# Performance work log

Hardware: AMD Instinct MI355X
Metric: run time of the kernel (lower is better)

Reference implementation:

```python
import jax, jax.numpy as jnp
import numpy as np

HIDDEN = 2048
NUM_HEADS = 16
HEAD_DIM = HIDDEN // NUM_HEADS
BATCH, SEQ = 2, 2048


def setup_inputs() -> dict:
    key = jax.random.key(0)
    ks = jax.random.split(key, 9)
    s = 1.0 / np.sqrt(HIDDEN)
    return {
        "hidden_state": jax.random.normal(ks[0], (BATCH, SEQ, HIDDEN), dtype=jnp.float32),
        "Wq": jax.random.normal(ks[1], (HIDDEN, HIDDEN), dtype=jnp.float32) * s,
        "bq": jax.random.normal(ks[2], (HIDDEN,), dtype=jnp.float32) * 0.01,
        "Wk": jax.random.normal(ks[3], (HIDDEN, HIDDEN), dtype=jnp.float32) * s,
        "bk": jax.random.normal(ks[4], (HIDDEN,), dtype=jnp.float32) * 0.01,
        "Wv": jax.random.normal(ks[5], (HIDDEN, HIDDEN), dtype=jnp.float32) * s,
        "bv": jax.random.normal(ks[6], (HIDDEN,), dtype=jnp.float32) * 0.01,
        "Wo": jax.random.normal(ks[7], (HIDDEN, HIDDEN), dtype=jnp.float32) * s,
        "bo": jax.random.normal(ks[8], (HIDDEN,), dtype=jnp.float32) * 0.01,
    }


def _split_heads(x):
    # (B, S, H*D) -> (B, H, S, D)
    b, s, _ = x.shape
    return x.reshape(b, s, NUM_HEADS, HEAD_DIM).transpose(0, 2, 1, 3)


def reference(hidden_state, Wq, bq, Wk, bk, Wv, bv, Wo, bo):
    q = _split_heads(hidden_state @ Wq + bq)
    k = _split_heads(hidden_state @ Wk + bk)
    v = _split_heads(hidden_state @ Wv + bv)
    scale = 1.0 / jnp.sqrt(jnp.asarray(HEAD_DIM, dtype=hidden_state.dtype))
    scores = jnp.einsum("bhqd,bhkd->bhqk", q, k) * scale  # (B,H,S,S)
    probs = jax.nn.softmax(scores, axis=-1)
    out = jnp.einsum("bhqk,bhkd->bhqd", probs, v)  # (B,H,S,D)
    b, h, s, d = out.shape
    out = out.transpose(0, 2, 1, 3).reshape(b, s, h * d)  # merge heads
    return out @ Wo + bo
```

## Files before the change

### kernel.cpp

```cpp
#include <hip/hip_runtime.h>
#include <math.h>

typedef __bf16 bf16;
typedef __bf16 bf16x4 __attribute__((ext_vector_type(4)));
typedef __bf16 bf16x8 __attribute__((ext_vector_type(8)));
typedef float  f32x4  __attribute__((ext_vector_type(4)));

#define HIDDEN 2048
#define NH     16
#define HD     128
#define BATCH  2
#define SEQ    2048
#define MROWS  (BATCH*SEQ)
#define NQKV   (3*HIDDEN)

__device__ __forceinline__ void async16(const bf16* g, bf16* l) {
  __builtin_amdgcn_global_load_lds(
      (const __attribute__((address_space(1))) void*)g,
      (__attribute__((address_space(3))) void*)l, 16, 0, 0);
}

__global__ __launch_bounds__(256) void cast_f32_bf16_kernel(
    const float* __restrict__ src, bf16* __restrict__ dst, int n4) {
  int i = blockIdx.x * 256 + threadIdx.x;
  if (i >= n4) return;
  float4 f = ((const float4*)src)[i];
  bf16x4 o;
  o[0] = (bf16)f.x; o[1] = (bf16)f.y; o[2] = (bf16)f.z; o[3] = (bf16)f.w;
  ((bf16x4*)dst)[i] = o;
}

__global__ __launch_bounds__(256) void transpose_cast_kernel(
    const float* __restrict__ src, bf16* __restrict__ dst) {
  __shared__ float t[32][33];
  int x  = blockIdx.x * 32 + threadIdx.x;
  int y0 = blockIdx.y * 32;
#pragma unroll
  for (int i = 0; i < 32; i += 8)
    t[threadIdx.y + i][threadIdx.x] = src[(size_t)(y0 + threadIdx.y + i) * HIDDEN + x];
  __syncthreads();
  int xo  = blockIdx.y * 32 + threadIdx.x;
  int yo0 = blockIdx.x * 32;
#pragma unroll
  for (int i = 0; i < 32; i += 8)
    dst[(size_t)(yo0 + threadIdx.y + i) * HIDDEN + xo] = (bf16)t[threadIdx.x][threadIdx.y + i];
}

__global__ __launch_bounds__(256) void concat3_kernel(
    const float* __restrict__ a, const float* __restrict__ b,
    const float* __restrict__ c, float* __restrict__ dst) {
  int i = blockIdx.x * 256 + threadIdx.x;
  float v = (i < 2048) ? a[i] : (i < 4096 ? b[i - 2048] : c[i - 4096]);
  dst[i] = v;
}

__global__ __launch_bounds__(256) void transpose_v_kernel(
    const bf16* __restrict__ QKV, bf16* __restrict__ Vt) {
  __shared__ bf16 t[32][33];
  int bh = blockIdx.z, b = bh >> 4, h = bh & 15;
  const bf16* src = QKV + (size_t)b * SEQ * NQKV + 2 * HIDDEN + h * HD;
  bf16* dst = Vt + (size_t)bh * HD * SEQ;
  int s0 = blockIdx.x * 32, d0 = blockIdx.y * 32;
#pragma unroll
  for (int i = 0; i < 32; i += 8)
    t[threadIdx.y + i][threadIdx.x] = src[(size_t)(s0 + threadIdx.y + i) * NQKV + d0 + threadIdx.x];
  __syncthreads();
#pragma unroll
  for (int i = 0; i < 32; i += 8)
    dst[(size_t)(d0 + threadIdx.y + i) * SEQ + s0 + threadIdx.x] = t[threadIdx.x][threadIdx.y + i];
}

template <typename OutT>
__global__ __launch_bounds__(256) void gemm_bt_bias(
    const bf16* __restrict__ A, const bf16* __restrict__ Bt,
    const float* __restrict__ bias, OutT* __restrict__ C, int N, int K) {
  __shared__ bf16 Ash[128 * 32];
  __shared__ bf16 Bsh[128 * 32];
  const int tid = threadIdx.x;
  const int wave = tid >> 6, lane = tid & 63, quad = lane >> 4, l16 = lane & 15;
  const int wm = (wave & 1) * 64, wn = (wave >> 1) * 64;
  const int m0 = blockIdx.x * 128, n0 = blockIdx.y * 128;
  (void)lane;

  const f32x4 zero4 = {0.f, 0.f, 0.f, 0.f};
  f32x4 acc[4][4];
#pragma unroll
  for (int i = 0; i < 4; i++)
#pragma unroll
    for (int j = 0; j < 4; j++) acc[i][j] = zero4;

  const int crow = tid >> 2, ccc = tid & 3;

  for (int kt = 0; kt < K; kt += 32) {
    __syncthreads();
    async16(&A[(size_t)(m0 + crow) * K + kt + ccc * 8],       &Ash[crow * 32 + ccc * 8]);
    async16(&A[(size_t)(m0 + crow + 64) * K + kt + ccc * 8],  &Ash[(crow + 64) * 32 + ccc * 8]);
    async16(&Bt[(size_t)(n0 + crow) * K + kt + ccc * 8],      &Bsh[crow * 32 + ccc * 8]);
    async16(&Bt[(size_t)(n0 + crow + 64) * K + kt + ccc * 8], &Bsh[(crow + 64) * 32 + ccc * 8]);
    __syncthreads();

    bf16x8 af[4], bfr[4];
#pragma unroll
    for (int i = 0; i < 4; i++) af[i]  = *(const bf16x8*)&Ash[(wm + i * 16 + l16) * 32 + quad * 8];
#pragma unroll
    for (int j = 0; j < 4; j++) bfr[j] = *(const bf16x8*)&Bsh[(wn + j * 16 + l16) * 32 + quad * 8];
#pragma unroll
    for (int i = 0; i < 4; i++)
#pragma unroll
      for (int j = 0; j < 4; j++)
        acc[i][j] = __builtin_amdgcn_mfma_f32_16x16x32_bf16(af[i], bfr[j], acc[i][j], 0, 0, 0);
  }

#pragma unroll
  for (int i = 0; i < 4; i++)
#pragma unroll
    for (int j = 0; j < 4; j++) {
      int n = n0 + wn + j * 16 + l16;
      float bv = bias[n];
#pragma unroll
      for (int r = 0; r < 4; r++) {
        int m = m0 + wm + i * 16 + quad * 4 + r;
        C[(size_t)m * N + n] = (OutT)(acc[i][j][r] + bv);
      }
    }
}

#define KTS   64
#define PPAD  72

__global__ __launch_bounds__(256, 2) void flash_attn_kernel(
    const bf16* __restrict__ QKV, const bf16* __restrict__ Vt, bf16* __restrict__ O) {
  const int bh = blockIdx.y, b = bh >> 4, h = bh & 15;
  const int q0 = blockIdx.x * 128;
  const int tid = threadIdx.x, wave = tid >> 6, lane = tid & 63, quad = lane >> 4, l16 = lane & 15;

  const bf16* Qb  = QKV + (size_t)b * SEQ * NQKV + h * HD;
  const bf16* Kb  = QKV + (size_t)b * SEQ * NQKV + HIDDEN + h * HD;
  const bf16* Vtb = Vt + (size_t)bh * HD * SEQ;

  __shared__ bf16 Ksh[KTS * HD];
  __shared__ bf16 Vsh[HD * KTS];
  __shared__ bf16 Psh[128 * PPAD];

  const int qrow = q0 + wave * 32;
  const float sc = 0.08838834764831845f * 1.44269504088896340f;

  bf16x8 qf[2][4];
#pragma unroll
  for (int mt = 0; mt < 2; mt++)
#pragma unroll
    for (int kk = 0; kk < 4; kk++) {
      bf16x8 t = *(const bf16x8*)&Qb[(size_t)(qrow + mt * 16 + l16) * NQKV + kk * 32 + quad * 8];
#pragma unroll
      for (int j = 0; j < 8; j++) t[j] = (bf16)((float)t[j] * sc);
      qf[mt][kk] = t;
    }

  const f32x4 zero4 = {0.f, 0.f, 0.f, 0.f};
  f32x4 oacc[2][8];
#pragma unroll
  for (int mt = 0; mt < 2; mt++)
#pragma unroll
    for (int nt = 0; nt < 8; nt++) oacc[mt][nt] = zero4;

  float lrun[2][4];
#pragma unroll
  for (int mt = 0; mt < 2; mt++)
#pragma unroll
    for (int r = 0; r < 4; r++) lrun[mt][r] = 0.f;

  const int krp = tid >> 4, kpp = tid & 15;
  const int vrp = tid >> 3, vpp = tid & 7;
  const int l7 = l16 & 7;

  for (int kt = 0; kt < SEQ; kt += KTS) {
    __syncthreads();
#pragma unroll
    for (int s = 0; s < 4; s++) {
      int r  = s * 16 + krp;
      int c  = kpp ^ (r & 7);
      async16(&Kb[(size_t)(kt + r) * NQKV + c * 8], &Ksh[s * 2048 + tid * 8]);
      int rv = s * 32 + vrp;
      int cv = vpp ^ (rv & 7);
      async16(&Vtb[(size_t)rv * SEQ + kt + cv * 8], &Vsh[s * 2048 + tid * 8]);
    }
    __syncthreads();

    f32x4 sacc[2][4];
#pragma unroll
    for (int mt = 0; mt < 2; mt++)
#pragma unroll
      for (int nt = 0; nt < 4; nt++) sacc[mt][nt] = zero4;
#pragma unroll
    for (int kk = 0; kk < 4; kk++) {
      bf16x8 kf[4];
#pragma unroll
      for (int nt = 0; nt < 4; nt++) {
        int p = (4 * kk + quad) ^ l7;
        kf[nt] = *(const bf16x8*)&Ksh[(nt * 16 + l16) * HD + p * 8];
      }
#pragma unroll
      for (int mt = 0; mt < 2; mt++)
#pragma unroll
        for (int nt = 0; nt < 4; nt++)
          sacc[mt][nt] = __builtin_amdgcn_mfma_f32_16x16x32_bf16(qf[mt][kk], kf[nt], sacc[mt][nt], 0, 0, 0);
    }

    float rs[2][4] = {};
#pragma unroll
    for (int mt = 0; mt < 2; mt++)
#pragma unroll
      for (int nt = 0; nt < 4; nt++)
#pragma unroll
        for (int r = 0; r < 4; r++) {
          float p = exp2f(sacc[mt][nt][r]);
          rs[mt][r] += p;
          Psh[(wave * 32 + mt * 16 + quad * 4 + r) * PPAD + nt * 16 + l16] = (bf16)p;
        }
#pragma unroll
    for (int mt = 0; mt < 2; mt++)
#pragma unroll
      for (int r = 0; r < 4; r++) {
        float t = rs[mt][r];
        t += __shfl_xor(t, 1);
        t += __shfl_xor(t, 2);
        t += __shfl_xor(t, 4);
        t += __shfl_xor(t, 8);
        lrun[mt][r] += t;
      }

#pragma unroll
    for (int kk2 = 0; kk2 < 2; kk2++) {
      bf16x8 pf[2], vf[8];
#pragma unroll
      for (int mt = 0; mt < 2; mt++)
        pf[mt] = *(const bf16x8*)&Psh[(wave * 32 + mt * 16 + l16) * PPAD + kk2 * 32 + quad * 8];
#pragma unroll
      for (int nt = 0; nt < 8; nt++) {
        int p = (4 * kk2 + quad) ^ l7;
        vf[nt] = *(const bf16x8*)&Vsh[(nt * 16 + l16) * KTS + p * 8];
      }
#pragma unroll
      for (int mt = 0; mt < 2; mt++)
#pragma unroll
        for (int nt = 0; nt < 8; nt++)
          oacc[mt][nt] = __builtin_amdgcn_mfma_f32_16x16x32_bf16(pf[mt], vf[nt], oacc[mt][nt], 0, 0, 0);
    }
  }

#pragma unroll
  for (int mt = 0; mt < 2; mt++) {
    float inv[4];
#pragma unroll
    for (int r = 0; r < 4; r++) inv[r] = 1.0f / lrun[mt][r];
#pragma unroll
    for (int nt = 0; nt < 8; nt++)
#pragma unroll
      for (int r = 0; r < 4; r++) {
        int q = qrow + mt * 16 + quad * 4 + r;
        int d = nt * 16 + l16;
        O[(size_t)(b * SEQ + q) * HIDDEN + h * HD + d] = (bf16)(oacc[mt][nt][r] * inv[r]);
      }
  }
}

extern "C" void kernel_launch(void* const* d_in, const int* in_sizes, int n_in,
                              void* d_out, int out_size, void* d_ws, size_t ws_size,
                              hipStream_t stream) {
  const float* hs = (const float*)d_in[0];
  const float* Wq = (const float*)d_in[1];
  const float* bq = (const float*)d_in[2];
  const float* Wk = (const float*)d_in[3];
  const float* bk = (const float*)d_in[4];
  const float* Wv = (const float*)d_in[5];
  const float* bv = (const float*)d_in[6];
  const float* Wo = (const float*)d_in[7];
  const float* bo = (const float*)d_in[8];
  float* out = (float*)d_out;

  char* ws = (char*)d_ws;
  bf16*  Abf   = (bf16*)(ws);
  bf16*  WtQKV = (bf16*)(ws + 16777216);
  bf16*  WtO   = (bf16*)(ws + 41943040);
  float* biasQ = (float*)(ws + 50331648);
  bf16*  QKV   = (bf16*)(ws + 50356224);
  bf16*  VT    = (bf16*)(ws + 100687872);
  bf16*  Obf   = (bf16*)(ws + 117465088);

  dim3 tb(32, 8);
  cast_f32_bf16_kernel<<<8192, 256, 0, stream>>>(hs, Abf, 2097152);
  transpose_cast_kernel<<<dim3(64, 64), tb, 0, stream>>>(Wq, WtQKV);
  transpose_cast_kernel<<<dim3(64, 64), tb, 0, stream>>>(Wk, WtQKV + 2048 * 2048);
  transpose_cast_kernel<<<dim3(64, 64), tb, 0, stream>>>(Wv, WtQKV + 2 * 2048 * 2048);
  transpose_cast_kernel<<<dim3(64, 64), tb, 0, stream>>>(Wo, WtO);
  concat3_kernel<<<24, 256, 0, stream>>>(bq, bk, bv, biasQ);

  gemm_bt_bias<bf16><<<dim3(32, 48), 256, 0, stream>>>(Abf, WtQKV, biasQ, QKV, NQKV, HIDDEN);
  transpose_v_kernel<<<dim3(64, 4, 32), tb, 0, stream>>>(QKV, VT);
  flash_attn_kernel<<<dim3(16, 32), 256, 0, stream>>>(QKV, VT, Obf);
  gemm_bt_bias<float><<<dim3(32, 16), 256, 0, stream>>>(Obf, WtO, bo, out, HIDDEN, HIDDEN);
}
```

Before: 466.7 us.

## Use 32x32 MFMA with swizzled LDS in GEMM, XCD block mapping, smaller attention tiles

The GEMM switches from 16x16x32 to 32x32x16 MFMA tiles and XOR-swizzles the LDS layout to avoid bank conflicts. It also remaps the linear block index so each XCD handles a contiguous range of N-blocks for better L2 reuse. The flash attention kernel halves its query tile to 64 rows, one 16-row strip per wave, doubling the grid and raising occupancy to 3 blocks per CU. The four weight transpose launches are merged into one launch. The smaller attention tile means each loaded K/V tile is reused across fewer queries, which raises K/V load traffic.

New measurement: 483.2 us. 3.5% more time.

```diff
diff --git a/kernel.cpp b/kernel.cpp
--- a/kernel.cpp
+++ b/kernel.cpp
@@ -5,6 +5,7 @@
 typedef __bf16 bf16x4 __attribute__((ext_vector_type(4)));
 typedef __bf16 bf16x8 __attribute__((ext_vector_type(8)));
 typedef float  f32x4  __attribute__((ext_vector_type(4)));
+typedef float  f32x16 __attribute__((ext_vector_type(16)));
 
 #define HIDDEN 2048
 #define NH     16
@@ -30,8 +31,18 @@
   ((bf16x4*)dst)[i] = o;
 }
 
-__global__ __launch_bounds__(256) void transpose_cast_kernel(
-    const float* __restrict__ src, bf16* __restrict__ dst) {
+__global__ __launch_bounds__(256) void transpose_cast4_kernel(
+    const float* __restrict__ s0, const float* __restrict__ s1,
+    const float* __restrict__ s2, const float* __restrict__ s3,
+    bf16* __restrict__ d0, bf16* __restrict__ d1,
+    bf16* __restrict__ d2, bf16* __restrict__ d3) {
+  const float* src; bf16* dst;
+  switch (blockIdx.z) {
+    case 0: src = s0; dst = d0; break;
+    case 1: src = s1; dst = d1; break;
+    case 2: src = s2; dst = d2; break;
+    default: src = s3; dst = d3; break;
+  }
   __shared__ float t[32][33];
   int x  = blockIdx.x * 32 + threadIdx.x;
   int y0 = blockIdx.y * 32;
@@ -77,50 +88,63 @@
   __shared__ bf16 Ash[128 * 32];
   __shared__ bf16 Bsh[128 * 32];
   const int tid = threadIdx.x;
-  const int wave = tid >> 6, lane = tid & 63, quad = lane >> 4, l16 = lane & 15;
+  const int wave = tid >> 6, lane = tid & 63;
+  const int l32 = lane & 31, lhi = lane >> 5;
   const int wm = (wave & 1) * 64, wn = (wave >> 1) * 64;
-  const int m0 = blockIdx.x * 128, n0 = blockIdx.y * 128;
-  (void)lane;
-
-  const f32x4 zero4 = {0.f, 0.f, 0.f, 0.f};
-  f32x4 acc[4][4];
-#pragma unroll
-  for (int i = 0; i < 4; i++)
-#pragma unroll
-    for (int j = 0; j < 4; j++) acc[i][j] = zero4;
+
+  const int NB = N >> 7;
+  const int bid = blockIdx.x;
+  const int xcd = bid & 7, jj = bid >> 3;
+  const int nb = xcd * (NB >> 3) + (jj >> 5);
+  const int mb = jj & 31;
+  const int m0 = mb * 128, n0 = nb * 128;
+
+  f32x16 acc[2][2];
+#pragma unroll
+  for (int i = 0; i < 2; i++)
+#pragma unroll
+    for (int j = 0; j < 2; j++)
+#pragma unroll
+      for (int r = 0; r < 16; r++) acc[i][j][r] = 0.f;
 
   const int crow = tid >> 2, ccc = tid & 3;
+  const int cs = ccc ^ (crow & 3);
 
   for (int kt = 0; kt < K; kt += 32) {
     __syncthreads();
-    async16(&A[(size_t)(m0 + crow) * K + kt + ccc * 8],       &Ash[crow * 32 + ccc * 8]);
-    async16(&A[(size_t)(m0 + crow + 64) * K + kt + ccc * 8],  &Ash[(crow + 64) * 32 + ccc * 8]);
-    async16(&Bt[(size_t)(n0 + crow) * K + kt + ccc * 8],      &Bsh[crow * 32 + ccc * 8]);
-    async16(&Bt[(size_t)(n0 + crow + 64) * K + kt + ccc * 8], &Bsh[(crow + 64) * 32 + ccc * 8]);
-    __syncthreads();
-
-    bf16x8 af[4], bfr[4];
-#pragma unroll
-    for (int i = 0; i < 4; i++) af[i]  = *(const bf16x8*)&Ash[(wm + i * 16 + l16) * 32 + quad * 8];
-#pragma unroll
-    for (int j = 0; j < 4; j++) bfr[j] = *(const bf16x8*)&Bsh[(wn + j * 16 + l16) * 32 + quad * 8];
-#pragma unroll
-    for (int i = 0; i < 4; i++)
-#pragma unroll
-      for (int j = 0; j < 4; j++)
-        acc[i][j] = __builtin_amdgcn_mfma_f32_16x16x32_bf16(af[i], bfr[j], acc[i][j], 0, 0, 0);
-  }
-
-#pragma unroll
-  for (int i = 0; i < 4; i++)
-#pragma unroll
-    for (int j = 0; j < 4; j++) {
-      int n = n0 + wn + j * 16 + l16;
+    async16(&A[(size_t)(m0 + crow) * K + kt + cs * 8],       &Ash[tid * 8]);
+    async16(&A[(size_t)(m0 + crow + 64) * K + kt + cs * 8],  &Ash[2048 + tid * 8]);
+    async16(&Bt[(size_t)(n0 + crow) * K + kt + cs * 8],      &Bsh[tid * 8]);
+    async16(&Bt[(size_t)(n0 + crow + 64) * K + kt + cs * 8], &Bsh[2048 + tid * 8]);
+    __syncthreads();
+
+#pragma unroll
+    for (int s = 0; s < 2; s++) {
+      const int p = (s * 2 + lhi) ^ (l32 & 3);
+      bf16x8 af[2], bfr[2];
+#pragma unroll
+      for (int i = 0; i < 2; i++) {
+        af[i]  = *(const bf16x8*)&Ash[(wm + i * 32 + l32) * 32 + p * 8];
+        bfr[i] = *(const bf16x8*)&Bsh[(wn + i * 32 + l32) * 32 + p * 8];
+      }
+#pragma unroll
+      for (int i = 0; i < 2; i++)
+#pragma unroll
+        for (int j = 0; j < 2; j++)
+          acc[i][j] = __builtin_amdgcn_mfma_f32_32x32x16_bf16(af[i], bfr[j], acc[i][j], 0, 0, 0);
+    }
+  }
+
+#pragma unroll
+  for (int i = 0; i < 2; i++)
+#pragma unroll
+    for (int j = 0; j < 2; j++) {
+      int n = n0 + wn + j * 32 + l32;
       float bv = bias[n];
 #pragma unroll
-      for (int r = 0; r < 4; r++) {
-        int m = m0 + wm + i * 16 + quad * 4 + r;
-        C[(size_t)m * N + n] = (OutT)(acc[i][j][r] + bv);
+      for (int r = 0; r < 16; r++) {
+        int row = wm + i * 32 + (r & 3) + 8 * (r >> 2) + 4 * lhi;
+        C[(size_t)(m0 + row) * N + n] = (OutT)(acc[i][j][r] + bv);
       }
     }
 }
@@ -128,10 +152,10 @@
 #define KTS   64
 #define PPAD  72
 
-__global__ __launch_bounds__(256, 2) void flash_attn_kernel(
+__global__ __launch_bounds__(256, 3) void flash_attn_kernel(
     const bf16* __restrict__ QKV, const bf16* __restrict__ Vt, bf16* __restrict__ O) {
   const int bh = blockIdx.y, b = bh >> 4, h = bh & 15;
-  const int q0 = blockIdx.x * 128;
+  const int q0 = blockIdx.x * 64;
   const int tid = threadIdx.x, wave = tid >> 6, lane = tid & 63, quad = lane >> 4, l16 = lane & 15;
 
   const bf16* Qb  = QKV + (size_t)b * SEQ * NQKV + h * HD;
@@ -140,34 +164,25 @@
 
   __shared__ bf16 Ksh[KTS * HD];
   __shared__ bf16 Vsh[HD * KTS];
-  __shared__ bf16 Psh[128 * PPAD];
-
-  const int qrow = q0 + wave * 32;
+  __shared__ bf16 Psh[64 * PPAD];
+
+  const int qrow = q0 + wave * 16;
   const float sc = 0.08838834764831845f * 1.44269504088896340f;
 
-  bf16x8 qf[2][4];
-#pragma unroll
-  for (int mt = 0; mt < 2; mt++)
-#pragma unroll
-    for (int kk = 0; kk < 4; kk++) {
-      bf16x8 t = *(const bf16x8*)&Qb[(size_t)(qrow + mt * 16 + l16) * NQKV + kk * 32 + quad * 8];
-#pragma unroll
-      for (int j = 0; j < 8; j++) t[j] = (bf16)((float)t[j] * sc);
-      qf[mt][kk] = t;
-    }
+  bf16x8 qf[4];
+#pragma unroll
+  for (int kk = 0; kk < 4; kk++) {
+    bf16x8 t = *(const bf16x8*)&Qb[(size_t)(qrow + l16) * NQKV + kk * 32 + quad * 8];
+#pragma unroll
+    for (int j = 0; j < 8; j++) t[j] = (bf16)((float)t[j] * sc);
+    qf[kk] = t;
+  }
 
   const f32x4 zero4 = {0.f, 0.f, 0.f, 0.f};
-  f32x4 oacc[2][8];
-#pragma unroll
-  for (int mt = 0; mt < 2; mt++)
-#pragma unroll
-    for (int nt = 0; nt < 8; nt++) oacc[mt][nt] = zero4;
-
-  float lrun[2][4];
-#pragma unroll
-  for (int mt = 0; mt < 2; mt++)
-#pragma unroll
-    for (int r = 0; r < 4; r++) lrun[mt][r] = 0.f;
+  f32x4 oacc[8];
+#pragma unroll
+  for (int nt = 0; nt < 8; nt++) oacc[nt] = zero4;
+  float lrun[4] = {0.f, 0.f, 0.f, 0.f};
 
   const int krp = tid >> 4, kpp = tid & 15;
   const int vrp = tid >> 3, vpp = tid & 7;
@@ -186,82 +201,65 @@
     }
     __syncthreads();
 
-    f32x4 sacc[2][4];
-#pragma unroll
-    for (int mt = 0; mt < 2; mt++)
-#pragma unroll
-      for (int nt = 0; nt < 4; nt++) sacc[mt][nt] = zero4;
+    f32x4 sacc[4];
+#pragma unroll
+    for (int nt = 0; nt < 4; nt++) sacc[nt] = zero4;
 #pragma unroll
     for (int kk = 0; kk < 4; kk++) {
+      const int p = (4 * kk + quad) ^ l7;
       bf16x8 kf[4];
 #pragma unroll
-      for (int nt = 0; nt < 4; nt++) {
-        int p = (4 * kk + quad) ^ l7;
+      for (int nt = 0; nt < 4; nt++)
         kf[nt] = *(const bf16x8*)&Ksh[(nt * 16 + l16) * HD + p * 8];
+#pragma unroll
+      for (int nt = 0; nt < 4; nt++)
+        sacc[nt] = __builtin_amdgcn_mfma_f32_16x16x32_bf16(qf[kk], kf[nt], sacc[nt], 0, 0, 0);
+    }
+
+    float rs[4] = {0.f, 0.f, 0.f, 0.f};
+#pragma unroll
+    for (int nt = 0; nt < 4; nt++)
+#pragma unroll
+      for (int r = 0; r < 4; r++) {
+        float p = exp2f(sacc[nt][r]);
+        rs[r] += p;
+        Psh[(wave * 16 + quad * 4 + r) * PPAD + nt * 16 + l16] = (bf16)p;
       }
 #pragma unroll
-      for (int mt = 0; mt < 2; mt++)
-#pragma unroll
-        for (int nt = 0; nt < 4; nt++)
-          sacc[mt][nt] = __builtin_amdgcn_mfma_f32_16x16x32_bf16(qf[mt][kk], kf[nt], sacc[mt][nt], 0, 0, 0);
-    }
-
-    float rs[2][4] = {};
-#pragma unroll
-    for (int mt = 0; mt < 2; mt++)
-#pragma unroll
-      for (int nt = 0; nt < 4; nt++)
-#pragma unroll
-        for (int r = 0; r < 4; r++) {
-          float p = exp2f(sacc[mt][nt][r]);
-          rs[mt][r] += p;
-          Psh[(wave * 32 + mt * 16 + quad * 4 + r) * PPAD + nt * 16 + l16] = (bf16)p;
-        }
-#pragma unroll
-    for (int mt = 0; mt < 2; mt++)
-#pragma unroll
-      for (int r = 0; r < 4; r++) {
-        float t = rs[mt][r];
-        t += __shfl_xor(t, 1);
-        t += __shfl_xor(t, 2);
-        t += __shfl_xor(t, 4);
-        t += __shfl_xor(t, 8);
-        lrun[mt][r] += t;
-      }
+    for (int r = 0; r < 4; r++) {
+      float t = rs[r];
+      t += __shfl_xor(t, 1);
+      t += __shfl_xor(t, 2);
+      t += __shfl_xor(t, 4);
+      t += __shfl_xor(t, 8);
+      lrun[r] += t;
+    }
 
 #pragma unroll
     for (int kk2 = 0; kk2 < 2; kk2++) {
-      bf16x8 pf[2], vf[8];
-#pragma unroll
-      for (int mt = 0; mt < 2; mt++)
-        pf[mt] = *(const bf16x8*)&Psh[(wave * 32 + mt * 16 + l16) * PPAD + kk2 * 32 + quad * 8];
-#pragma unroll
-      for (int nt = 0; nt < 8; nt++) {
-        int p = (4 * kk2 + quad) ^ l7;
+      const int p = (4 * kk2 + quad) ^ l7;
+      bf16x8 pf, vf[8];
+      pf = *(const bf16x8*)&Psh[(wave * 16 + l16) * PPAD + kk2 * 32 + quad * 8];
+#pragma unroll
+      for (int nt = 0; nt < 8; nt++)
         vf[nt] = *(const bf16x8*)&Vsh[(nt * 16 + l16) * KTS + p * 8];
-      }
-#pragma unroll
-      for (int mt = 0; mt < 2; mt++)
-#pragma unroll
-        for (int nt = 0; nt < 8; nt++)
-          oacc[mt][nt] = __builtin_amdgcn_mfma_f32_16x16x32_bf16(pf[mt], vf[nt], oacc[mt][nt], 0, 0, 0);
-    }
-  }
-
-#pragma unroll
-  for (int mt = 0; mt < 2; mt++) {
-    float inv[4];
-#pragma unroll
-    for (int r = 0; r < 4; r++) inv[r] = 1.0f / lrun[mt][r];
-#pragma unroll
-    for (int nt = 0; nt < 8; nt++)
-#pragma unroll
-      for (int r = 0; r < 4; r++) {
-        int q = qrow + mt * 16 + quad * 4 + r;
-        int d = nt * 16 + l16;
-        O[(size_t)(b * SEQ + q) * HIDDEN + h * HD + d] = (bf16)(oacc[mt][nt][r] * inv[r]);
-      }
-  }
+#pragma unroll
+      for (int nt = 0; nt < 8; nt++)
+        oacc[nt] = __builtin_amdgcn_mfma_f32_16x16x32_bf16(pf, vf[nt], oacc[nt], 0, 0, 0);
+    }
+  }
+
+  float inv[4];
+#pragma unroll
+  for (int r = 0; r < 4; r++) inv[r] = 1.0f / lrun[r];
+#pragma unroll
+  for (int nt = 0; nt < 8; nt++)
+#pragma unroll
+    for (int r = 0; r < 4; r++) {
+      int q = qrow + quad * 4 + r;
+      int d = nt * 16 + l16;
+      O[(size_t)(b * SEQ + q) * HIDDEN + h * HD + d] = (bf16)(oacc[nt][r] * inv[r]);
+    }
 }
 
 extern "C" void kernel_launch(void* const* d_in, const int* in_sizes, int n_in,
@@ -289,14 +287,13 @@
 
   dim3 tb(32, 8);
   cast_f32_bf16_kernel<<<8192, 256, 0, stream>>>(hs, Abf, 2097152);
-  transpose_cast_kernel<<<dim3(64, 64), tb, 0, stream>>>(Wq, WtQKV);
-  transpose_cast_kernel<<<dim3(64, 64), tb, 0, stream>>>(Wk, WtQKV + 2048 * 2048);
-  transpose_cast_kernel<<<dim3(64, 64), tb, 0, stream>>>(Wv, WtQKV + 2 * 2048 * 2048);
-  transpose_cast_kernel<<<dim3(64, 64), tb, 0, stream>>>(Wo, WtO);
+  transpose_cast4_kernel<<<dim3(64, 64, 4), tb, 0, stream>>>(
+      Wq, Wk, Wv, Wo,
+      WtQKV, WtQKV + 2048 * 2048, WtQKV + 2 * 2048 * 2048, WtO);
   concat3_kernel<<<24, 256, 0, stream>>>(bq, bk, bv, biasQ);
 
-  gemm_bt_bias<bf16><<<dim3(32, 48), 256, 0, stream>>>(Abf, WtQKV, biasQ, QKV, NQKV, HIDDEN);
+  gemm_bt_bias<bf16><<<32 * 48, 256, 0, stream>>>(Abf, WtQKV, biasQ, QKV, NQKV, HIDDEN);
   transpose_v_kernel<<<dim3(64, 4, 32), tb, 0, stream>>>(QKV, VT);
-  flash_attn_kernel<<<dim3(16, 32), 256, 0, stream>>>(QKV, VT, Obf);
-  gemm_bt_bias<float><<<dim3(32, 16), 256, 0, stream>>>(Obf, WtO, bo, out, HIDDEN, HIDDEN);
-}
+  flash_attn_kernel<<<dim3(32, 32), 256, 0, stream>>>(QKV, VT, Obf);
+  gemm_bt_bias<float><<<32 * 16, 256, 0, stream>>>(Obf, WtO, bo, out, HIDDEN, HIDDEN);
+}
```
